# Kernel optimization log

Measured on AMD Instinct MI355X. Metric: run time of the kernel, lower is better.

Reference implementation:

```python
import jax, jax.numpy as jnp
import numpy as np


def setup_inputs() -> dict:
    key = jax.random.key(0)
    k1, k2, k3, k4 = jax.random.split(key, 4)
    B, S, P = 256, 8192, 16383
    preds = jax.random.normal(k1, (B, S, 2), dtype=jnp.float32)
    targets = jax.random.normal(k2, (B, S, 2), dtype=jnp.float32)
    path_i = jax.random.randint(k3, (B, P), 0, S, dtype=jnp.int64)
    path_j = jax.random.randint(k4, (B, P), 0, S, dtype=jnp.int64)
    return {"preds": preds, "targets": targets, "path_i": path_i, "path_j": path_j}


def reference(preds, targets, path_i, path_j):
    # preds, targets: (B, S, 2); path_i, path_j: (B, P) index arrays (ragged
    # warping paths flattened to dense per-batch index lists).
    B, S, _ = preds.shape
    # Gather pred[i] and target[j] along the sequence axis -> (B, P, 2)
    p = jnp.take_along_axis(preds, path_i[..., None], axis=1)
    t = jnp.take_along_axis(targets, path_j[..., None], axis=1)
    # L1 norm per (i, j) pair, summed over all pairs and batches
    loss = jnp.sum(jnp.abs(p - t))
    return loss / (B * S)
```

## Files before the change

### kernel.cpp

```cpp
#include <hip/hip_runtime.h>


#define BB 256
#define SS 8192
#define PP 16383
#define NT 1024
#define NIT 16

__global__ __launch_bounds__(NT, 4) void dtw_loss_kernel(
    const float* __restrict__ preds,
    const float* __restrict__ targets,
    const int* __restrict__ path_i,
    const int* __restrict__ path_j,
    float* __restrict__ partial)
{
    __shared__ float lds[4 * SS];
    __shared__ float wred[16];

    const int tid   = threadIdx.x;
    const int batch = blockIdx.x;
    const int wave  = tid >> 6;
    const int lane  = tid & 63;

    const char* pbase = (const char*)(preds   + (size_t)batch * SS * 2);
    const char* tbase = (const char*)(targets + (size_t)batch * SS * 2);
    const int* __restrict__ pi = path_i + (size_t)batch * PP;
    const int* __restrict__ pj = path_j + (size_t)batch * PP;

    #pragma unroll
    for (int u = 0; u < 4; ++u) {
        const int off = (wave * 4 + u) * 1024;
        __builtin_amdgcn_global_load_lds(
            (const __attribute__((address_space(1))) void*)(pbase + off + lane * 16),
            (__attribute__((address_space(3))) void*)((char*)lds + off),
            16, 0, 0);
        __builtin_amdgcn_global_load_lds(
            (const __attribute__((address_space(1))) void*)(tbase + off + lane * 16),
            (__attribute__((address_space(3))) void*)((char*)lds + 65536 + off),
            16, 0, 0);
    }

    unsigned pk[NIT];
    #pragma unroll
    for (int u = 0; u < NIT; ++u) {
        int k = u * NT + tid;
        if (u == NIT - 1) k = min(k, PP - 1);
        pk[u] = ((unsigned)pi[k]) | ((unsigned)pj[k] << 16);
    }
    #pragma unroll
    for (int u = 0; u < NIT; ++u)
        asm volatile("" : "+v"(pk[u]));

    __syncthreads();

    const float2* __restrict__ lp = (const float2*)lds;
    const float2* __restrict__ lt = (const float2*)(lds + 2 * SS);
    float acc = 0.0f;
    #pragma unroll
    for (int u = 0; u < NIT; ++u) {
        const unsigned i = pk[u] & 0xffffu;
        const unsigned j = pk[u] >> 16;
        const float2 a = lp[i];
        const float2 b = lt[j];
        const float d = fabsf(a.x - b.x) + fabsf(a.y - b.y);
        if (u < NIT - 1 || u * NT + tid < PP) acc += d;
    }

    #pragma unroll
    for (int off = 32; off > 0; off >>= 1)
        acc += __shfl_down(acc, off, 64);
    if (lane == 0) wred[wave] = acc;
    __syncthreads();
    if (tid < 16) {
        float s = wred[tid];
        s += __shfl_down(s, 8, 64);
        s += __shfl_down(s, 4, 64);
        s += __shfl_down(s, 2, 64);
        s += __shfl_down(s, 1, 64);
        if (tid == 0) partial[batch] = s;
    }
}

__global__ __launch_bounds__(64) void dtw_final_kernel(
    const float* __restrict__ partial, float* __restrict__ out)
{
    const float4 v = ((const float4*)partial)[threadIdx.x];
    float s = (v.x + v.y) + (v.z + v.w);
    #pragma unroll
    for (int off = 32; off > 0; off >>= 1)
        s += __shfl_down(s, off, 64);
    if (threadIdx.x == 0)
        out[0] = s * (1.0f / ((float)BB * (float)SS));
}

extern "C" void kernel_launch(void* const* d_in, const int* in_sizes, int n_in,
                              void* d_out, int out_size, void* d_ws, size_t ws_size,
                              hipStream_t stream) {
    const float* preds   = (const float*)d_in[0];
    const float* targets = (const float*)d_in[1];
    const int*   path_i  = (const int*)d_in[2];
    const int*   path_j  = (const int*)d_in[3];
    float* partial = (float*)d_ws;
    float* out     = (float*)d_out;

    dtw_loss_kernel<<<BB, NT, 0, stream>>>(preds, targets, path_i, path_j, partial);
    dtw_final_kernel<<<1, 64, 0, stream>>>(partial, out);
}
```

Baseline: 101.9 us.

## Split preds/targets staging into two phases with partial vmcnt waits

Global loads are reordered so preds go to LDS and path_i indices are fetched first, then targets and path_j are issued. A partial s_waitcnt vmcnt(20) plus a barrier lets the preds LDS gathers start while the targets and path_j loads are still in flight. The aim is to overlap the second half of the memory traffic with the first half of the LDS gather work. In exchange it costs more registers (separate index arrays and the ax/ay arrays) and an extra block barrier. Correctness depends on the hand-counted vmcnt matching the compiler's actual load order.

Measured after the change: 99.41 us. -2.5%, faster.

```diff
diff --git a/kernel.cpp b/kernel.cpp
--- a/kernel.cpp
+++ b/kernel.cpp
@@ -34,35 +34,69 @@
             (const __attribute__((address_space(1))) void*)(pbase + off + lane * 16),
             (__attribute__((address_space(3))) void*)((char*)lds + off),
             16, 0, 0);
+    }
+    __builtin_amdgcn_sched_barrier(0);
+
+    unsigned ii[NIT];
+    #pragma unroll
+    for (int u = 0; u < NIT; ++u) {
+        int k = u * NT + tid;
+        if (u == NIT - 1) k = min(k, PP - 1);
+        ii[u] = (unsigned)pi[k];
+    }
+    __builtin_amdgcn_sched_barrier(0);
+
+    #pragma unroll
+    for (int u = 0; u < 4; ++u) {
+        const int off = (wave * 4 + u) * 1024;
         __builtin_amdgcn_global_load_lds(
             (const __attribute__((address_space(1))) void*)(tbase + off + lane * 16),
             (__attribute__((address_space(3))) void*)((char*)lds + 65536 + off),
             16, 0, 0);
     }
+    __builtin_amdgcn_sched_barrier(0);
 
-    unsigned pk[NIT];
+    unsigned jj[NIT];
     #pragma unroll
     for (int u = 0; u < NIT; ++u) {
         int k = u * NT + tid;
         if (u == NIT - 1) k = min(k, PP - 1);
-        pk[u] = ((unsigned)pi[k]) | ((unsigned)pj[k] << 16);
+        jj[u] = (unsigned)pj[k];
+    }
+    __builtin_amdgcn_sched_barrier(0);
+
+    #pragma unroll
+    for (int u = 0; u < NIT; ++u)
+        asm volatile("" : "+v"(ii[u]));
+    asm volatile("s_waitcnt vmcnt(20)" ::: "memory");
+    __builtin_amdgcn_s_barrier();
+    __builtin_amdgcn_sched_barrier(0);
+
+    const float2* __restrict__ lp = (const float2*)lds;
+    const float2* __restrict__ lt = (const float2*)(lds + 2 * SS);
+    float ax[NIT], ay[NIT];
+    #pragma unroll
+    for (int u = 0; u < NIT; ++u) {
+        const float2 a = lp[ii[u]];
+        ax[u] = a.x; ay[u] = a.y;
     }
     #pragma unroll
     for (int u = 0; u < NIT; ++u)
-        asm volatile("" : "+v"(pk[u]));
+        asm volatile("" : "+v"(ax[u]), "+v"(ay[u]));
+    __builtin_amdgcn_sched_barrier(0);
 
-    __syncthreads();
+    #pragma unroll
+    for (int u = 0; u < NIT; ++u)
+        asm volatile("" : "+v"(jj[u]));
+    asm volatile("s_waitcnt vmcnt(0)" ::: "memory");
+    __builtin_amdgcn_s_barrier();
+    __builtin_amdgcn_sched_barrier(0);
 
-    const float2* __restrict__ lp = (const float2*)lds;
-    const float2* __restrict__ lt = (const float2*)(lds + 2 * SS);
     float acc = 0.0f;
     #pragma unroll
     for (int u = 0; u < NIT; ++u) {
-        const unsigned i = pk[u] & 0xffffu;
-        const unsigned j = pk[u] >> 16;
-        const float2 a = lp[i];
-        const float2 b = lt[j];
-        const float d = fabsf(a.x - b.x) + fabsf(a.y - b.y);
+        const float2 b = lt[jj[u]];
+        const float d = fabsf(ax[u] - b.x) + fabsf(ay[u] - b.y);
         if (u < NIT - 1 || u * NT + tid < PP) acc += d;
     }
 
```
